# Optimization experiments

Hardware: AMD Instinct MI355X
Metric: run time of the kernel (lower is better)

## Reference

```python
import jax, jax.numpy as jnp
import numpy as np

THETA = 10000.0

def _rope(t):
    # lucidrains-style interleaved rotary over the FULL last dim (dim=hidden_size)
    T, d = t.shape[-2], t.shape[-1]
    freqs = 1.0 / (THETA ** (jnp.arange(0, d, 2, dtype=jnp.float32) / d))  # (d/2,)
    ang = jnp.arange(T, dtype=jnp.float32)[:, None] * freqs[None, :]       # (T, d/2)
    ang = jnp.repeat(ang, 2, axis=-1)                                      # (T, d) interleaved
    cos, sin = jnp.cos(ang), jnp.sin(ang)
    x = t.reshape(t.shape[:-1] + (d // 2, 2))
    x1, x2 = x[..., 0], x[..., 1]
    rot = jnp.stack([-x2, x1], axis=-1).reshape(t.shape)  # rotate_half, interleaved pairs
    return t * cos + rot * sin


def setup_inputs() -> dict:
    key = jax.random.key(0)
    ks = jax.random.split(key, 5)
    B, T, C = 4, 2048, 1024
    s = 0.02
    return {
        "x":  jax.random.normal(ks[0], (B, T, C), dtype=jnp.float32),
        "Wq": jax.random.normal(ks[1], (C, C), dtype=jnp.float32) * s,
        "bq": jnp.zeros((C,), dtype=jnp.float32),
        "Wk": jax.random.normal(ks[2], (C, C), dtype=jnp.float32) * s,
        "bk": jnp.zeros((C,), dtype=jnp.float32),
        "Wv": jax.random.normal(ks[3], (C, C), dtype=jnp.float32) * s,
        "bv": jnp.zeros((C,), dtype=jnp.float32),
        "Wf": jax.random.normal(ks[4], (C, C), dtype=jnp.float32) * s,
        "bf": jnp.zeros((C,), dtype=jnp.float32),
    }


def reference(x, Wq, bq, Wk, bk, Wv, bv, Wf, bf):
    B, T, C = x.shape
    Q = _rope(x @ Wq.T + bq)
    K = _rope(x @ Wk.T + bk)
    V = x @ Wv.T + bv
    # scores [B,T,T]; _get_D(gamma=1, T) is exactly a causal lower-triangular mask
    A = jnp.einsum('btd,bsd->bts', Q, K) / jnp.sqrt(jnp.float32(C))
    causal = jnp.tril(jnp.ones((T, T), dtype=bool))
    A = jnp.where(causal, A, -jnp.inf)
    A = jax.nn.softmax(A, axis=-1)
    out = jnp.einsum('bts,bsd->btd', A, V)
    return out @ Wf.T + bf
```

## Files before the change

kernel.cpp:

```cpp
#include <hip/hip_runtime.h>
#include <math.h>


#define AS1(p) ((__attribute__((address_space(1))) void*)(p))
#define AS3(p) ((__attribute__((address_space(3))) void*)(p))

typedef __attribute__((ext_vector_type(8))) short bf16x8;
typedef __attribute__((ext_vector_type(4))) float f32x4;

__device__ __forceinline__ unsigned short f2bf(float f) {
  unsigned int u = __float_as_uint(f);
  u += 0x7fffu + ((u >> 16) & 1u);
  return (unsigned short)(u >> 16);
}

__global__ __launch_bounds__(256) void cast_all(
    const float* __restrict__ x, const float* __restrict__ Wq,
    const float* __restrict__ Wk, const float* __restrict__ Wv,
    const float* __restrict__ Wf,
    unsigned short* __restrict__ xb, unsigned short* __restrict__ Wqb,
    unsigned short* __restrict__ Wkb, unsigned short* __restrict__ Wvb,
    unsigned short* __restrict__ Wfb) {
  int i = blockIdx.x * 256 + threadIdx.x;
  const float* src; unsigned short* dst; int off;
  if (i < 2097152) { src = x; dst = xb; off = i; }
  else {
    int j = i - 2097152;
    int w = j >> 18; off = j & 262143;
    src = (w == 0) ? Wq : (w == 1) ? Wk : (w == 2) ? Wv : Wf;
    dst = (w == 0) ? Wqb : (w == 1) ? Wkb : (w == 2) ? Wvb : Wfb;
  }
  float4 f = ((const float4*)src)[off];
  ushort4 o;
  o.x = f2bf(f.x); o.y = f2bf(f.y); o.z = f2bf(f.z); o.w = f2bf(f.w);
  ((ushort4*)dst)[off] = o;
}

__device__ __forceinline__ void gemm_core(const unsigned short* __restrict__ At, long long lda,
                                          const unsigned short* __restrict__ Bt, long long ldb,
                                          int K, f32x4 (&acc)[4][4],
                                          unsigned short* As, unsigned short* Bs) {
  const int tid  = threadIdx.x;
  const int lane = tid & 63;
  const int w    = tid >> 6;
  const int wm   = (w & 1) << 6;
  const int wn   = (w >> 1) << 6;
  const int fr   = lane & 15;
  const int fq   = lane >> 4;
  const int srow = tid >> 2;
  const int scol = (tid & 3) << 3;
  const int lg   = ((tid & 3) ^ ((srow >> 1) & 3)) << 3;
  const unsigned short* a0 = At + (long long)srow * lda + lg;
  const unsigned short* a1 = At + (long long)(srow + 64) * lda + lg;
  const unsigned short* b0 = Bt + (long long)srow * ldb + lg;
  const unsigned short* b1 = Bt + (long long)(srow + 64) * ldb + lg;
  unsigned short* As0 = As + srow * 32 + scol;
  unsigned short* As1 = As + (srow + 64) * 32 + scol;
  unsigned short* Bs0 = Bs + srow * 32 + scol;
  unsigned short* Bs1 = Bs + (srow + 64) * 32 + scol;
  const int pg = (fq ^ ((fr >> 1) & 3)) << 3;
  for (int k0 = 0; k0 < K; k0 += 32) {
    __builtin_amdgcn_global_load_lds(AS1(a0 + k0), AS3(As0), 16, 0, 0);
    __builtin_amdgcn_global_load_lds(AS1(a1 + k0), AS3(As1), 16, 0, 0);
    __builtin_amdgcn_global_load_lds(AS1(b0 + k0), AS3(Bs0), 16, 0, 0);
    __builtin_amdgcn_global_load_lds(AS1(b1 + k0), AS3(Bs1), 16, 0, 0);
    __syncthreads();
    bf16x8 af[4], bfr[4];
#pragma unroll
    for (int i = 0; i < 4; i++)
      af[i] = *(const bf16x8*)(As + (wm + i * 16 + fr) * 32 + pg);
#pragma unroll
    for (int i = 0; i < 4; i++)
      bfr[i] = *(const bf16x8*)(Bs + (wn + i * 16 + fr) * 32 + pg);
#pragma unroll
    for (int mi = 0; mi < 4; mi++)
#pragma unroll
      for (int ni = 0; ni < 4; ni++)
        acc[mi][ni] = __builtin_amdgcn_mfma_f32_16x16x32_bf16(af[mi], bfr[ni], acc[mi][ni], 0, 0, 0);
    __syncthreads();
  }
}

__device__ __forceinline__ void repack_store_mi(unsigned short (&vals)[4][4],
                                                unsigned short* sh, int mi,
                                                int m0, int n0, long long ldo,
                                                unsigned short* __restrict__ Out) {
  const int tid = threadIdx.x, lane = tid & 63, w = tid >> 6;
  const int half = w & 1, wn = (w >> 1) << 6;
  const int cl = lane & 15, q4 = lane >> 4;
  const int lr = half * 16 + q4 * 4;
#pragma unroll
  for (int ni = 0; ni < 4; ni++)
#pragma unroll
    for (int rr = 0; rr < 4; rr++)
      sh[(lr + rr) * 132 + wn + ni * 16 + cl] = vals[ni][rr];
  __syncthreads();
#pragma unroll
  for (int it = 0; it < 2; ++it) {
    int row = (tid >> 4) + it * 16;
    int c8 = (tid & 15) << 3;
    bf16x8 v = *(const bf16x8*)(sh + row * 132 + c8);
    int gr = m0 + (row < 16 ? mi * 16 + row : 48 + mi * 16 + row);
    *(bf16x8*)(Out + (long long)gr * ldo + n0 + c8) = v;
  }
  __syncthreads();
}

__device__ __forceinline__ void core8(
    const unsigned short* __restrict__ A, long long lda,
    const unsigned short* __restrict__ B, long long ldb,
    int nkt, f32x4 (&acc)[4][4], unsigned short* lds) {
  const int tid  = threadIdx.x;
  const int lane = tid & 63;
  const int w    = tid >> 6;
  const int wr   = w >> 2;
  const int wc   = w & 3;
  const int fr   = lane & 15;
  const int fq   = lane >> 4;
  const int rsw0 = (fq ^ (fr & 7)) << 3;
  const int rsw1 = ((4 + fq) ^ (fr & 7)) << 3;
  const int sr   = tid >> 3;
  const int kswz = ((tid & 7) ^ (sr & 7)) << 3;
  const unsigned short* Asrc = A + (long long)sr * lda + kswz;
  const unsigned short* Bsrc = B + (long long)sr * ldb + kswz;
  unsigned short* ldsw = lds + tid * 8;

  auto stageA = [&](int b_, int kt_) {
    const unsigned short* s0 = Asrc + (long long)kt_ * 64;
    __builtin_amdgcn_global_load_lds(AS1(s0),            AS3(ldsw + b_ * 24576),         16, 0, 0);
    __builtin_amdgcn_global_load_lds(AS1(s0 + 64 * lda), AS3(ldsw + b_ * 24576 + 4096),  16, 0, 0);
  };
  auto stageB = [&](int b_, int kt_) {
    const unsigned short* s0 = Bsrc + (long long)kt_ * 64;
    __builtin_amdgcn_global_load_lds(AS1(s0),             AS3(ldsw + b_ * 24576 + 8192),  16, 0, 0);
    __builtin_amdgcn_global_load_lds(AS1(s0 + 64 * ldb),  AS3(ldsw + b_ * 24576 + 12288), 16, 0, 0);
    __builtin_amdgcn_global_load_lds(AS1(s0 + 128 * ldb), AS3(ldsw + b_ * 24576 + 16384), 16, 0, 0);
    __builtin_amdgcn_global_load_lds(AS1(s0 + 192 * ldb), AS3(ldsw + b_ * 24576 + 20480), 16, 0, 0);
  };

  stageA(0, 0); stageB(0, 0);
  if (nkt > 1) {
    stageA(1, 1); stageB(1, 1);
    asm volatile("s_waitcnt vmcnt(6)" ::: "memory");
  } else {
    asm volatile("s_waitcnt vmcnt(0)" ::: "memory");
  }
  __builtin_amdgcn_s_barrier();

  const unsigned short* Ar = lds + (wr * 64 + fr) * 64;
  const unsigned short* Br = lds + 8192 + (wc * 64 + fr) * 64;

#define MFMA2(ACC, A0, A1, B0, B1)                                            \
  ACC = __builtin_amdgcn_mfma_f32_16x16x32_bf16(A0, B0, ACC, 0, 0, 0);        \
  ACC = __builtin_amdgcn_mfma_f32_16x16x32_bf16(A1, B1, ACC, 0, 0, 0);

#pragma unroll 1
  for (int kt = 0; kt < nkt; ++kt) {
    const int b = kt & 1;
    const unsigned short* Ab = Ar + b * 24576;
    const unsigned short* Bb = Br + b * 24576;
    bf16x8 aL[4], aH[4], bE[4], bO[4];
    aL[0] = *(const bf16x8*)(Ab + rsw0);
    aL[1] = *(const bf16x8*)(Ab + rsw1);
    aL[2] = *(const bf16x8*)(Ab + 1024 + rsw0);
    aL[3] = *(const bf16x8*)(Ab + 1024 + rsw1);
    bE[0] = *(const bf16x8*)(Bb + rsw0);
    bE[1] = *(const bf16x8*)(Bb + rsw1);
    bE[2] = *(const bf16x8*)(Bb + 1024 + rsw0);
    bE[3] = *(const bf16x8*)(Bb + 1024 + rsw1);
    __builtin_amdgcn_s_barrier();
    asm volatile("s_waitcnt lgkmcnt(0)" ::: "memory");
    __builtin_amdgcn_s_setprio(1);
    MFMA2(acc[0][0], aL[0], aL[1], bE[0], bE[1]);
    MFMA2(acc[0][1], aL[0], aL[1], bE[2], bE[3]);
    MFMA2(acc[1][0], aL[2], aL[3], bE[0], bE[1]);
    MFMA2(acc[1][1], aL[2], aL[3], bE[2], bE[3]);
    __builtin_amdgcn_s_setprio(0);
    __builtin_amdgcn_s_barrier();
    bO[0] = *(const bf16x8*)(Bb + 2048 + rsw0);
    bO[1] = *(const bf16x8*)(Bb + 2048 + rsw1);
    bO[2] = *(const bf16x8*)(Bb + 3072 + rsw0);
    bO[3] = *(const bf16x8*)(Bb + 3072 + rsw1);
    __builtin_amdgcn_s_barrier();
    asm volatile("s_waitcnt lgkmcnt(0)" ::: "memory");
    __builtin_amdgcn_s_setprio(1);
    MFMA2(acc[0][2], aL[0], aL[1], bO[0], bO[1]);
    MFMA2(acc[0][3], aL[0], aL[1], bO[2], bO[3]);
    MFMA2(acc[1][2], aL[2], aL[3], bO[0], bO[1]);
    MFMA2(acc[1][3], aL[2], aL[3], bO[2], bO[3]);
    __builtin_amdgcn_s_setprio(0);
    __builtin_amdgcn_s_barrier();
    aH[0] = *(const bf16x8*)(Ab + 2048 + rsw0);
    aH[1] = *(const bf16x8*)(Ab + 2048 + rsw1);
    aH[2] = *(const bf16x8*)(Ab + 3072 + rsw0);
    aH[3] = *(const bf16x8*)(Ab + 3072 + rsw1);
    if (kt + 2 < nkt) stageB(b, kt + 2);
    __builtin_amdgcn_s_barrier();
    asm volatile("s_waitcnt lgkmcnt(0)" ::: "memory");
    __builtin_amdgcn_s_setprio(1);
    MFMA2(acc[2][0], aH[0], aH[1], bE[0], bE[1]);
    MFMA2(acc[2][1], aH[0], aH[1], bE[2], bE[3]);
    MFMA2(acc[3][0], aH[2], aH[3], bE[0], bE[1]);
    MFMA2(acc[3][1], aH[2], aH[3], bE[2], bE[3]);
    __builtin_amdgcn_s_setprio(0);
    __builtin_amdgcn_s_barrier();
    if (kt + 2 < nkt) stageA(b, kt + 2);
    if (kt + 1 < nkt) {
      if (kt + 2 < nkt)
        asm volatile("s_waitcnt vmcnt(6)" ::: "memory");
      else
        asm volatile("s_waitcnt vmcnt(0)" ::: "memory");
    }
    __builtin_amdgcn_s_barrier();
    __builtin_amdgcn_s_setprio(1);
    MFMA2(acc[2][2], aH[0], aH[1], bO[0], bO[1]);
    MFMA2(acc[2][3], aH[0], aH[1], bO[2], bO[3]);
    MFMA2(acc[3][2], aH[2], aH[3], bO[0], bO[1]);
    MFMA2(acc[3][3], aH[2], aH[3], bO[2], bO[3]);
    __builtin_amdgcn_s_setprio(0);
    __builtin_amdgcn_s_barrier();
  }
#undef MFMA2
}

__global__ __launch_bounds__(512, 2) void proj_rope(
    const unsigned short* __restrict__ xb,
    const unsigned short* __restrict__ Wq, const unsigned short* __restrict__ Wk,
    const unsigned short* __restrict__ Wv,
    const float* __restrict__ bq, const float* __restrict__ bk, const float* __restrict__ bv,
    unsigned short* __restrict__ Q, unsigned short* __restrict__ Ko,
    unsigned short* __restrict__ Vt) {
  __shared__ unsigned short lds[49152];
  const int which = blockIdx.z;
  const int tid = threadIdx.x, lane = tid & 63, w = tid >> 6;
  const int wr = w >> 2, wc = w & 3;
  const int cl = lane & 15, q4 = lane >> 4;

  f32x4 acc[4][4];
#pragma unroll
  for (int i = 0; i < 4; i++)
#pragma unroll
    for (int j = 0; j < 4; j++)
#pragma unroll
      for (int k = 0; k < 4; k++) acc[i][j][k] = 0.0f;

  if (which == 2) {
    const int flat = blockIdx.x * 4 + blockIdx.y;
    const int m0 = (flat & 7) * 128;
    const int n0 = (flat >> 3) * 256;
    core8(Wv + (long long)m0 * 1024, 1024, xb + (long long)n0 * 1024, 1024, 16, acc, lds);
    __syncthreads();
    const int b = n0 >> 11, sloc = n0 & 2047;
#pragma unroll
    for (int mi = 0; mi < 4; ++mi) {
      const int lr = wr * 64 + mi * 16 + q4 * 4;
#pragma unroll
      for (int rr = 0; rr < 4; ++rr) {
        const float b_ = bv[m0 + lr + rr];
#pragma unroll
        for (int nj = 0; nj < 4; ++nj)
          lds[(lr + rr) * 264 + wc * 64 + nj * 16 + cl] = f2bf(acc[mi][nj][rr] + b_);
      }
    }
    __syncthreads();
    unsigned short* Outb = Vt + (long long)b * 1024 * 2048;
#pragma unroll
    for (int it = 0; it < 8; ++it) {
      int c = it * 512 + tid;
      int row = c >> 5, c8 = (c & 31) << 3;
      bf16x8 v = *(const bf16x8*)(lds + row * 264 + c8);
      *(bf16x8*)(Outb + (long long)(m0 + row) * 2048 + sloc + c8) = v;
    }
    return;
  }

  const int m0 = blockIdx.x * 128;
  const int n0 = blockIdx.y * 256;
  const unsigned short* W = which == 0 ? Wq : Wk;
  const float* bias = which == 0 ? bq : bk;
  unsigned short* Out = which == 0 ? Q : Ko;

  core8(xb + (long long)m0 * 1024, 1024, W + (long long)n0 * 1024, 1024, 16, acc, lds);
  __syncthreads();

  const float NEG_L2T_512 = -0.025952563239354392f;
  const float INV2PI = 0.15915494309189535f;
  float freqn[4];
#pragma unroll
  for (int nj = 0; nj < 4; ++nj) {
    int gn = n0 + wc * 64 + nj * 16 + cl;
    freqn[nj] = exp2f(NEG_L2T_512 * (float)(gn >> 1));
  }
#pragma unroll
  for (int mi = 0; mi < 4; ++mi) {
    const int lr = wr * 64 + mi * 16 + q4 * 4;
    const int t0 = (m0 & 2047) + lr;
#pragma unroll
    for (int nj = 0; nj < 4; ++nj) {
      const int gn = n0 + wc * 64 + nj * 16 + cl;
      const float bi = bias[gn];
#pragma unroll
      for (int rr = 0; rr < 4; ++rr) {
        float v = acc[mi][nj][rr] + bi;
        float partner = __shfl_xor(v, 1, 64);
        float ang = (float)(t0 + rr) * freqn[nj];
        float rev = ang * INV2PI;
        rev = rev - floorf(rev);
        float c_ = __builtin_amdgcn_cosf(rev);
        float s_ = __builtin_amdgcn_sinf(rev);
        v = v * c_ + ((gn & 1) ? partner : -partner) * s_;
        lds[(lr + rr) * 264 + wc * 64 + nj * 16 + cl] = f2bf(v);
      }
    }
  }
  __syncthreads();
#pragma unroll
  for (int it = 0; it < 8; ++it) {
    int c = it * 512 + tid;
    int row = c >> 5, c8 = (c & 31) << 3;
    bf16x8 v = *(const bf16x8*)(lds + row * 264 + c8);
    *(bf16x8*)(Out + (long long)(m0 + row) * 1024 + n0 + c8) = v;
  }
}

__global__ __launch_bounds__(256) void score_exp(const unsigned short* __restrict__ Q,
                                                 const unsigned short* __restrict__ Kk,
                                                 unsigned short* __restrict__ P,
                                                 float* __restrict__ row_sum) {
  __shared__ unsigned short sh[8192];
  const int bx = blockIdx.x;
  int i = (int)((sqrtf(8.0f * (float)bx + 1.0f) - 1.0f) * 0.5f);
  while ((i + 1) * (i + 2) / 2 <= bx) ++i;
  while (i * (i + 1) / 2 > bx) --i;
  const int j = bx - i * (i + 1) / 2;
  const int b = blockIdx.z;
  const int m0 = i * 128, n0 = j * 128;
  const unsigned short* Qb = Q + (long long)b * 2048 * 1024;
  const unsigned short* Kb = Kk + (long long)b * 2048 * 1024;
  unsigned short* Pb = P + (long long)b * 2048 * 2048;
  float* rs = row_sum + b * 2048;

  f32x4 acc[4][4];
#pragma unroll
  for (int ii = 0; ii < 4; ii++)
#pragma unroll
    for (int jj = 0; jj < 4; jj++)
#pragma unroll
      for (int k = 0; k < 4; k++) acc[ii][jj][k] = 0.0f;

  gemm_core(Qb + (long long)m0 * 1024, 1024, Kb + (long long)n0 * 1024, 1024, 1024, acc, sh, sh + 4096);

  const int tid = threadIdx.x, lane = tid & 63, w = tid >> 6;
  const int wm = (w & 1) << 6, wn = (w >> 1) << 6;
  const int cl = lane & 15, q4 = lane >> 4;
  const bool diag = (i == j);
#pragma unroll
  for (int mi = 0; mi < 4; mi++) {
    unsigned short vals[4][4];
    float rsum[4] = {0.f, 0.f, 0.f, 0.f};
#pragma unroll
    for (int ni = 0; ni < 4; ni++) {
      const int gn = n0 + wn + ni * 16 + cl;
#pragma unroll
      for (int rr = 0; rr < 4; rr++) {
        const int gm = m0 + wm + mi * 16 + q4 * 4 + rr;
        float e = (diag && gn > gm) ? 0.0f : __expf(acc[mi][ni][rr] * 0.03125f);
        vals[ni][rr] = f2bf(e);
        rsum[rr] += e;
      }
    }
#pragma unroll
    for (int rr = 0; rr < 4; rr++) {
#pragma unroll
      for (int off = 1; off < 16; off <<= 1) rsum[rr] += __shfl_xor(rsum[rr], off, 64);
    }
    if (cl == 0) {
      const int gm = m0 + wm + mi * 16 + q4 * 4;
#pragma unroll
      for (int rr = 0; rr < 4; rr++) atomicAdd(&rs[gm + rr], rsum[rr]);
    }
    repack_store_mi(vals, sh, mi, m0, n0, 2048, Pb);
  }
}

__global__ __launch_bounds__(256) void pv_gemm(const unsigned short* __restrict__ P,
                                               const unsigned short* __restrict__ Vt,
                                               const float* __restrict__ row_sum,
                                               unsigned short* __restrict__ O) {
  __shared__ unsigned short sh[8192];
  const int b = blockIdx.z;
  const int mt = 15 - blockIdx.x;
  const int m0 = mt * 128;
  const int n0 = blockIdx.y * 128;
  const unsigned short* Pb = P + (long long)b * 2048 * 2048;
  const unsigned short* Vb = Vt + (long long)b * 1024 * 2048;
  const float* rs = row_sum + b * 2048;
  const int K = m0 + 128;

  f32x4 acc[4][4];
#pragma unroll
  for (int i = 0; i < 4; i++)
#pragma unroll
    for (int j = 0; j < 4; j++)
#pragma unroll
      for (int k = 0; k < 4; k++) acc[i][j][k] = 0.0f;

  gemm_core(Pb + (long long)m0 * 2048, 2048, Vb + (long long)n0 * 2048, 2048, K, acc, sh, sh + 4096);

  const int tid = threadIdx.x, lane = tid & 63, w = tid >> 6;
  const int wm = (w & 1) << 6;
  const int q4 = lane >> 4;
#pragma unroll
  for (int mi = 0; mi < 4; mi++) {
    unsigned short vals[4][4];
    float inv[4];
    const int gm0 = m0 + wm + mi * 16 + q4 * 4;
#pragma unroll
    for (int rr = 0; rr < 4; rr++) inv[rr] = 1.0f / rs[gm0 + rr];
#pragma unroll
    for (int ni = 0; ni < 4; ni++)
#pragma unroll
      for (int rr = 0; rr < 4; rr++)
        vals[ni][rr] = f2bf(acc[mi][ni][rr] * inv[rr]);
    repack_store_mi(vals, sh, mi, m0, n0, 1024, O + (long long)b * 2048 * 1024);
  }
}

__global__ __launch_bounds__(512, 2) void final_gemm(const unsigned short* __restrict__ O,
                                                     const unsigned short* __restrict__ Wf,
                                                     const float* __restrict__ bf_,
                                                     float* __restrict__ out) {
  __shared__ unsigned short lds[49152];
  float* shf = (float*)lds;
  const int tid = threadIdx.x, lane = tid & 63, w = tid >> 6;
  const int wr = w >> 2, wc = w & 3;
  const int cl = lane & 15, q4 = lane >> 4;
  const int m0 = blockIdx.x * 128;
  const int n0 = blockIdx.y * 256;

  f32x4 acc[4][4];
#pragma unroll
  for (int i = 0; i < 4; i++)
#pragma unroll
    for (int j = 0; j < 4; j++)
#pragma unroll
      for (int k = 0; k < 4; k++) acc[i][j][k] = 0.0f;

  core8(O + (long long)m0 * 1024, 1024, Wf + (long long)n0 * 1024, 1024, 16, acc, lds);

#pragma unroll
  for (int r = 0; r < 2; ++r) {
    __syncthreads();
    if (wr == r) {
#pragma unroll
      for (int mi = 0; mi < 4; ++mi)
#pragma unroll
        for (int nj = 0; nj < 4; ++nj) {
          const int col = wc * 64 + nj * 16 + cl;
          const float bi = bf_[n0 + col];
#pragma unroll
          for (int rr = 0; rr < 4; ++rr)
            shf[(mi * 16 + q4 * 4 + rr) * 260 + col] = acc[mi][nj][rr] + bi;
        }
    }
    __syncthreads();
#pragma unroll
    for (int it = 0; it < 8; ++it) {
      int c = it * 512 + tid;
      int row = c >> 6, c4 = (c & 63) << 2;
      float4 v = *(const float4*)(shf + row * 260 + c4);
      *(float4*)(out + (long long)(m0 + r * 64 + row) * 1024 + n0 + c4) = v;
    }
  }
}

extern "C" void kernel_launch(void* const* d_in, const int* in_sizes, int n_in,
                              void* d_out, int out_size, void* d_ws, size_t ws_size,
                              hipStream_t stream) {
  (void)in_sizes; (void)n_in; (void)out_size; (void)ws_size;
  const float* x   = (const float*)d_in[0];
  const float* Wq  = (const float*)d_in[1];
  const float* bq  = (const float*)d_in[2];
  const float* Wk  = (const float*)d_in[3];
  const float* bk  = (const float*)d_in[4];
  const float* Wv  = (const float*)d_in[5];
  const float* bv  = (const float*)d_in[6];
  const float* Wf  = (const float*)d_in[7];
  const float* bf_ = (const float*)d_in[8];
  float* out = (float*)d_out;

  char* ws = (char*)d_ws;
  const size_t MB = 1024 * 1024;
  unsigned short* xb  = (unsigned short*)(ws);
  unsigned short* Wqb = (unsigned short*)(ws + 16 * MB);
  unsigned short* Wkb = (unsigned short*)(ws + 18 * MB);
  unsigned short* Wvb = (unsigned short*)(ws + 20 * MB);
  unsigned short* Wfb = (unsigned short*)(ws + 22 * MB);
  unsigned short* Qb  = (unsigned short*)(ws + 24 * MB);
  unsigned short* Kb  = (unsigned short*)(ws + 40 * MB);
  unsigned short* Vtb = (unsigned short*)(ws + 56 * MB);
  unsigned short* Ob  = (unsigned short*)(ws + 72 * MB);
  unsigned short* Pb  = (unsigned short*)(ws + 88 * MB);
  float*          rsum= (float*)(ws + 120 * MB);

  hipMemsetAsync(rsum, 0, 8192 * sizeof(float), stream);
  cast_all<<<dim3(3145728 / 256), dim3(256), 0, stream>>>(x, Wq, Wk, Wv, Wf, xb, Wqb, Wkb, Wvb, Wfb);
  proj_rope<<<dim3(64, 4, 3), dim3(512), 0, stream>>>(xb, Wqb, Wkb, Wvb, bq, bk, bv, Qb, Kb, Vtb);
  score_exp<<<dim3(136, 1, 4), dim3(256), 0, stream>>>(Qb, Kb, Pb, rsum);
  pv_gemm<<<dim3(16, 8, 4), dim3(256), 0, stream>>>(Pb, Vtb, rsum, Ob);
  final_gemm<<<dim3(64, 4), dim3(512), 0, stream>>>(Ob, Wfb, bf_, out);
}
```

Before: 293.0 us.

## Restructure GEMM core into half-K stages with 32-wide swizzled LDS layout

Reworks the bf16 GEMM inner loop so each 64-wide K tile is split into two 32-wide halves. Each half is staged into LDS separately with a new XOR swizzle on a 32-element row pitch, and each half feeds a full 4x4 MFMA block from one set of fragment loads. Global-to-LDS prefetches are now issued per half, interleaved with the compute phases, and there are two barrier-separated phases per tile instead of four. The aim is fewer LDS reads and barriers per tile and finer-grained overlap of loads with MFMA, at the cost of a tighter vmcnt schedule and a new LDS layout that must match the readers.

```diff
diff --git a/kernel.cpp b/kernel.cpp
--- a/kernel.cpp
+++ b/kernel.cpp
@@ -117,110 +117,91 @@
   const int wc   = w & 3;
   const int fr   = lane & 15;
   const int fq   = lane >> 4;
-  const int rsw0 = (fq ^ (fr & 7)) << 3;
-  const int rsw1 = ((4 + fq) ^ (fr & 7)) << 3;
-  const int sr   = tid >> 3;
-  const int kswz = ((tid & 7) ^ (sr & 7)) << 3;
-  const unsigned short* Asrc = A + (long long)sr * lda + kswz;
-  const unsigned short* Bsrc = B + (long long)sr * ldb + kswz;
-  unsigned short* ldsw = lds + tid * 8;
-
-  auto stageA = [&](int b_, int kt_) {
-    const unsigned short* s0 = Asrc + (long long)kt_ * 64;
-    __builtin_amdgcn_global_load_lds(AS1(s0),            AS3(ldsw + b_ * 24576),         16, 0, 0);
-    __builtin_amdgcn_global_load_lds(AS1(s0 + 64 * lda), AS3(ldsw + b_ * 24576 + 4096),  16, 0, 0);
-  };
-  auto stageB = [&](int b_, int kt_) {
-    const unsigned short* s0 = Bsrc + (long long)kt_ * 64;
-    __builtin_amdgcn_global_load_lds(AS1(s0),             AS3(ldsw + b_ * 24576 + 8192),  16, 0, 0);
-    __builtin_amdgcn_global_load_lds(AS1(s0 + 64 * ldb),  AS3(ldsw + b_ * 24576 + 12288), 16, 0, 0);
-    __builtin_amdgcn_global_load_lds(AS1(s0 + 128 * ldb), AS3(ldsw + b_ * 24576 + 16384), 16, 0, 0);
-    __builtin_amdgcn_global_load_lds(AS1(s0 + 192 * ldb), AS3(ldsw + b_ * 24576 + 20480), 16, 0, 0);
-  };
-
-  stageA(0, 0); stageB(0, 0);
+  const int csel = (fq ^ ((fr >> 1) & 3)) << 3;
+  const int srow = tid >> 2;
+  const int scsw = ((tid & 3) ^ ((srow >> 1) & 3)) << 3;
+  const unsigned short* Asrc  = A + (long long)srow * lda + scsw;
+  const unsigned short* Bsrc0 = B + (long long)srow * ldb + scsw;
+  const unsigned short* Bsrc1 = B + (long long)(srow + 128) * ldb + scsw;
+  unsigned short* dst0 = lds + tid * 8;
+
+#define STAGE(b_, kt_, h_)                                                       \
+  do {                                                                           \
+    const int ko_ = (kt_) * 64 + (h_) * 32;                                      \
+    __builtin_amdgcn_global_load_lds(AS1(Asrc + ko_),                            \
+        AS3(dst0 + (b_) * 24576 + (h_) * 4096), 16, 0, 0);                       \
+    __builtin_amdgcn_global_load_lds(AS1(Bsrc0 + ko_),                           \
+        AS3(dst0 + (b_) * 24576 + 8192 + (h_) * 8192), 16, 0, 0);                \
+    __builtin_amdgcn_global_load_lds(AS1(Bsrc1 + ko_),                           \
+        AS3(dst0 + (b_) * 24576 + 8192 + (h_) * 8192 + 4096), 16, 0, 0);         \
+  } while (0)
+
+  STAGE(0, 0, 0);
+  STAGE(0, 0, 1);
   if (nkt > 1) {
-    stageA(1, 1); stageB(1, 1);
+    STAGE(1, 1, 0);
     asm volatile("s_waitcnt vmcnt(6)" ::: "memory");
   } else {
-    asm volatile("s_waitcnt vmcnt(0)" ::: "memory");
+    asm volatile("s_waitcnt vmcnt(3)" ::: "memory");
   }
   __builtin_amdgcn_s_barrier();
-
-  const unsigned short* Ar = lds + (wr * 64 + fr) * 64;
-  const unsigned short* Br = lds + 8192 + (wc * 64 + fr) * 64;
-
-#define MFMA2(ACC, A0, A1, B0, B1)                                            \
-  ACC = __builtin_amdgcn_mfma_f32_16x16x32_bf16(A0, B0, ACC, 0, 0, 0);        \
-  ACC = __builtin_amdgcn_mfma_f32_16x16x32_bf16(A1, B1, ACC, 0, 0, 0);
+  __builtin_amdgcn_sched_barrier(0);
+
+  const unsigned short* Ard = lds + (wr * 64 + fr) * 32 + csel;
+  const unsigned short* Brd = lds + 8192 + (wc * 64 + fr) * 32 + csel;
 
 #pragma unroll 1
   for (int kt = 0; kt < nkt; ++kt) {
-    const int b = kt & 1;
-    const unsigned short* Ab = Ar + b * 24576;
-    const unsigned short* Bb = Br + b * 24576;
-    bf16x8 aL[4], aH[4], bE[4], bO[4];
-    aL[0] = *(const bf16x8*)(Ab + rsw0);
-    aL[1] = *(const bf16x8*)(Ab + rsw1);
-    aL[2] = *(const bf16x8*)(Ab + 1024 + rsw0);
-    aL[3] = *(const bf16x8*)(Ab + 1024 + rsw1);
-    bE[0] = *(const bf16x8*)(Bb + rsw0);
-    bE[1] = *(const bf16x8*)(Bb + rsw1);
-    bE[2] = *(const bf16x8*)(Bb + 1024 + rsw0);
-    bE[3] = *(const bf16x8*)(Bb + 1024 + rsw1);
+    const int bo = (kt & 1) * 24576;
+    const unsigned short* Ab = Ard + bo;
+    const unsigned short* Bb = Brd + bo;
+    bf16x8 af[4], bf[4];
+#pragma unroll
+    for (int mi = 0; mi < 4; ++mi) af[mi] = *(const bf16x8*)(Ab + mi * 512);
+#pragma unroll
+    for (int nj = 0; nj < 4; ++nj) bf[nj] = *(const bf16x8*)(Bb + nj * 512);
+    if (kt + 1 < nkt) {
+      STAGE((kt + 1) & 1, kt + 1, 1);
+      asm volatile("s_waitcnt vmcnt(6)" ::: "memory");
+    } else {
+      asm volatile("s_waitcnt vmcnt(0)" ::: "memory");
+    }
     __builtin_amdgcn_s_barrier();
     asm volatile("s_waitcnt lgkmcnt(0)" ::: "memory");
+    __builtin_amdgcn_sched_barrier(0);
     __builtin_amdgcn_s_setprio(1);
-    MFMA2(acc[0][0], aL[0], aL[1], bE[0], bE[1]);
-    MFMA2(acc[0][1], aL[0], aL[1], bE[2], bE[3]);
-    MFMA2(acc[1][0], aL[2], aL[3], bE[0], bE[1]);
-    MFMA2(acc[1][1], aL[2], aL[3], bE[2], bE[3]);
+#pragma unroll
+    for (int mi = 0; mi < 4; ++mi)
+#pragma unroll
+      for (int nj = 0; nj < 4; ++nj)
+        acc[mi][nj] = __builtin_amdgcn_mfma_f32_16x16x32_bf16(af[mi], bf[nj], acc[mi][nj], 0, 0, 0);
     __builtin_amdgcn_s_setprio(0);
     __builtin_amdgcn_s_barrier();
-    bO[0] = *(const bf16x8*)(Bb + 2048 + rsw0);
-    bO[1] = *(const bf16x8*)(Bb + 2048 + rsw1);
-    bO[2] = *(const bf16x8*)(Bb + 3072 + rsw0);
-    bO[3] = *(const bf16x8*)(Bb + 3072 + rsw1);
+    __builtin_amdgcn_sched_barrier(0);
+#pragma unroll
+    for (int mi = 0; mi < 4; ++mi) af[mi] = *(const bf16x8*)(Ab + 4096 + mi * 512);
+#pragma unroll
+    for (int nj = 0; nj < 4; ++nj) bf[nj] = *(const bf16x8*)(Bb + 8192 + nj * 512);
+    if (kt + 2 < nkt) {
+      STAGE(kt & 1, kt + 2, 0);
+      asm volatile("s_waitcnt vmcnt(6)" ::: "memory");
+    } else if (kt + 1 < nkt) {
+      asm volatile("s_waitcnt vmcnt(3)" ::: "memory");
+    }
     __builtin_amdgcn_s_barrier();
     asm volatile("s_waitcnt lgkmcnt(0)" ::: "memory");
+    __builtin_amdgcn_sched_barrier(0);
     __builtin_amdgcn_s_setprio(1);
-    MFMA2(acc[0][2], aL[0], aL[1], bO[0], bO[1]);
-    MFMA2(acc[0][3], aL[0], aL[1], bO[2], bO[3]);
-    MFMA2(acc[1][2], aL[2], aL[3], bO[0], bO[1]);
-    MFMA2(acc[1][3], aL[2], aL[3], bO[2], bO[3]);
+#pragma unroll
+    for (int mi = 0; mi < 4; ++mi)
+#pragma unroll
+      for (int nj = 0; nj < 4; ++nj)
+        acc[mi][nj] = __builtin_amdgcn_mfma_f32_16x16x32_bf16(af[mi], bf[nj], acc[mi][nj], 0, 0, 0);
     __builtin_amdgcn_s_setprio(0);
     __builtin_amdgcn_s_barrier();
-    aH[0] = *(const bf16x8*)(Ab + 2048 + rsw0);
-    aH[1] = *(const bf16x8*)(Ab + 2048 + rsw1);
-    aH[2] = *(const bf16x8*)(Ab + 3072 + rsw0);
-    aH[3] = *(const bf16x8*)(Ab + 3072 + rsw1);
-    if (kt + 2 < nkt) stageB(b, kt + 2);
-    __builtin_amdgcn_s_barrier();
-    asm volatile("s_waitcnt lgkmcnt(0)" ::: "memory");
-    __builtin_amdgcn_s_setprio(1);
-    MFMA2(acc[2][0], aH[0], aH[1], bE[0], bE[1]);
-    MFMA2(acc[2][1], aH[0], aH[1], bE[2], bE[3]);
-    MFMA2(acc[3][0], aH[2], aH[3], bE[0], bE[1]);
-    MFMA2(acc[3][1], aH[2], aH[3], bE[2], bE[3]);
-    __builtin_amdgcn_s_setprio(0);
-    __builtin_amdgcn_s_barrier();
-    if (kt + 2 < nkt) stageA(b, kt + 2);
-    if (kt + 1 < nkt) {
-      if (kt + 2 < nkt)
-        asm volatile("s_waitcnt vmcnt(6)" ::: "memory");
-      else
-        asm volatile("s_waitcnt vmcnt(0)" ::: "memory");
-    }
-    __builtin_amdgcn_s_barrier();
-    __builtin_amdgcn_s_setprio(1);
-    MFMA2(acc[2][2], aH[0], aH[1], bO[0], bO[1]);
-    MFMA2(acc[2][3], aH[0], aH[1], bO[2], bO[3]);
-    MFMA2(acc[3][2], aH[2], aH[3], bO[0], bO[1]);
-    MFMA2(acc[3][3], aH[2], aH[3], bO[2], bO[3]);
-    __builtin_amdgcn_s_setprio(0);
-    __builtin_amdgcn_s_barrier();
-  }
-#undef MFMA2
+    __builtin_amdgcn_sched_barrier(0);
+  }
+#undef STAGE
 }
 
 __global__ __launch_bounds__(512, 2) void proj_rope(
```

Result: no change. 290.2 us (-1.0%).
